# Kernel tuning notes

Hardware: AMD Instinct MI355X
Metric: run time of the kernel (lower is better)

Reference implementation:

```python
import jax, jax.numpy as jnp
import numpy as np

D = 1024
H = 16
HD = D // H


def setup_inputs() -> dict:
    key = jax.random.key(0)
    ks = jax.random.split(key, 13)
    s = 0.02
    inp = {
        "x": jax.random.normal(ks[0], (2, 2048, D), dtype=jnp.float32),
        "Wq": jax.random.normal(ks[1], (D, D), dtype=jnp.float32) * s,
        "bq": jnp.zeros((D,), jnp.float32),
        "Wk": jax.random.normal(ks[2], (D, D), dtype=jnp.float32) * s,
        "bk": jnp.zeros((D,), jnp.float32),
        "Wv": jax.random.normal(ks[3], (D, D), dtype=jnp.float32) * s,
        "bv": jnp.zeros((D,), jnp.float32),
        "Wo": jax.random.normal(ks[4], (D, D), dtype=jnp.float32) * s,
        "bo": jnp.zeros((D,), jnp.float32),
        "W1": jax.random.normal(ks[5], (D, 4 * D), dtype=jnp.float32) * s,
        "b1": jnp.zeros((4 * D,), jnp.float32),
        "W2": jax.random.normal(ks[6], (4 * D, D), dtype=jnp.float32) * s,
        "b2": jnp.zeros((D,), jnp.float32),
    }
    return inp


def reference(x, Wq, bq, Wk, bk, Wv, bv, Wo, bo, W1, b1, W2, b2):
    B, L, _ = x.shape
    # attention (dropout = identity in eval); note: original forward never applies norm1/norm2
    q = (x @ Wq + bq).reshape(B, L, H, HD).transpose(0, 2, 1, 3)  # [B,H,L,HD]
    k = (x @ Wk + bk).reshape(B, L, H, HD).transpose(0, 2, 1, 3)
    v = (x @ Wv + bv).reshape(B, L, H, HD).transpose(0, 2, 1, 3)
    s = jnp.einsum("bhqd,bhkd->bhqk", q, k) / jnp.sqrt(jnp.float32(HD))
    causal = jnp.tril(jnp.ones((L, L), dtype=bool))
    s = jnp.where(causal[None, None, :, :], s, -jnp.inf)
    p = jax.nn.softmax(s, axis=-1)
    y = jnp.einsum("bhqk,bhkd->bhqd", p, v)
    y = y.transpose(0, 2, 1, 3).reshape(B, L, D)
    x = x + (y @ Wo + bo)
    # MLP with SiLU
    h = jax.nn.silu(x @ W1 + b1)
    x = x + (h @ W2 + b2)
    return x
```

## Files before the change

### kernel.cpp

```cpp
#include <hip/hip_runtime.h>
#include <hip/hip_bf16.h>
#include <stdint.h>

using u16 = unsigned short;
typedef __bf16 bf16x8 __attribute__((ext_vector_type(8)));
typedef float f32x4 __attribute__((ext_vector_type(4)));
typedef u16 u16x8 __attribute__((ext_vector_type(8)));

__device__ __forceinline__ float bf2f(u16 u) {
  union { unsigned int i; float f; } v; v.i = ((unsigned int)u) << 16; return v.f;
}
__device__ __forceinline__ u16 f2bf(float f) {
  __bf16 h = (__bf16)f;
  return __builtin_bit_cast(u16, h);
}
__device__ __forceinline__ float fexp2(float x) {
  return __builtin_amdgcn_exp2f(x);
}

__device__ __forceinline__ void gload_lds16(const void* g, void* l) {
  __builtin_amdgcn_global_load_lds(
      (__attribute__((address_space(1))) const void*)g,
      (__attribute__((address_space(3))) void*)l, 16, 0, 0);
}

__global__ void cvt_f32_bf16(const float* __restrict__ in, u16* __restrict__ out) {
  int i = (blockIdx.x * 256 + threadIdx.x) * 8;
  float4 a = *(const float4*)(in + i);
  float4 b = *(const float4*)(in + i + 4);
  u16x8 o;
  o[0] = f2bf(a.x); o[1] = f2bf(a.y); o[2] = f2bf(a.z); o[3] = f2bf(a.w);
  o[4] = f2bf(b.x); o[5] = f2bf(b.y); o[6] = f2bf(b.z); o[7] = f2bf(b.w);
  *(u16x8*)(out + i) = o;
}

__global__ void transpose_cvt(const float* __restrict__ W, u16* __restrict__ Wt,
                              int K, int N) {
  __shared__ float t[32][33];
  const int tx = threadIdx.x & 31, ty = threadIdx.x >> 5;
  const int n0 = blockIdx.x * 32, k0 = blockIdx.y * 32;
#pragma unroll
  for (int i = 0; i < 32; i += 8)
    t[ty + i][tx] = W[(size_t)(k0 + ty + i) * N + n0 + tx];
  __syncthreads();
#pragma unroll
  for (int i = 0; i < 32; i += 8)
    Wt[(size_t)(n0 + ty + i) * K + k0 + tx] = f2bf(t[tx][ty + i]);
}

__global__ void transpose_cvt4(const float* __restrict__ Wa, const float* __restrict__ Wb,
                               const float* __restrict__ Wc, const float* __restrict__ Wd,
                               u16* __restrict__ Da, u16* __restrict__ Db,
                               u16* __restrict__ Dc, u16* __restrict__ Dd) {
  __shared__ float t[32][33];
  const int z = blockIdx.z;
  const float* W = (z == 0) ? Wa : (z == 1) ? Wb : (z == 2) ? Wc : Wd;
  u16* D = (z == 0) ? Da : (z == 1) ? Db : (z == 2) ? Dc : Dd;
  const int tx = threadIdx.x & 31, ty = threadIdx.x >> 5;
  const int n0 = blockIdx.x * 32, k0 = blockIdx.y * 32;
#pragma unroll
  for (int i = 0; i < 32; i += 8)
    t[ty + i][tx] = W[(size_t)(k0 + ty + i) * 1024 + n0 + tx];
  __syncthreads();
#pragma unroll
  for (int i = 0; i < 32; i += 8)
    D[(size_t)(n0 + ty + i) * 1024 + k0 + tx] = f2bf(t[tx][ty + i]);
}

__global__ void transpose_v(const u16* __restrict__ qkv, u16* __restrict__ vt) {
  __shared__ u16 tile[32][34];
  const int tx = threadIdx.x & 31, ty = threadIdx.x >> 5;
  const int kv0 = blockIdx.x * 32, d0 = blockIdx.y * 32;
  const int bh = blockIdx.z, b = bh >> 4, h = bh & 15;
#pragma unroll
  for (int i = 0; i < 32; i += 8)
    tile[ty + i][tx] = qkv[(size_t)(b * 2048 + kv0 + ty + i) * 3072 + 2048 + h * 64 + d0 + tx];
  __syncthreads();
#pragma unroll
  for (int i = 0; i < 32; i += 8)
    vt[((size_t)bh * 64 + d0 + ty + i) * 2048 + kv0 + tx] = tile[tx][ty + i];
}

__global__ void concat_bias(const float* __restrict__ bq, const float* __restrict__ bk,
                            const float* __restrict__ bv, float* __restrict__ o) {
  int i = blockIdx.x * 256 + threadIdx.x;
  o[i] = (i < 1024) ? bq[i] : (i < 2048 ? bk[i - 1024] : bv[i - 2048]);
}

template <int EPI>
__global__ __launch_bounds__(512, 2) void gemm256_kernel(
    const u16* __restrict__ A, const u16* __restrict__ Bt,
    const float* __restrict__ bias, u16* __restrict__ outb,
    int M, int N, int K) {
  __shared__ u16 As[4][8192];
  __shared__ u16 Bs[4][8192];
  const int t = threadIdx.x;
  const int w = t >> 6, lane = t & 63, lr = lane & 15, lg = lane >> 4;
  const int wm = w >> 2, wn = w & 3;
  const int gx = gridDim.x;
  const int nwg = gx * gridDim.y;
  const int p = blockIdx.y * gx + blockIdx.x;
  const int L = (p & 7) * (nwg >> 3) + (p >> 3);
  const int m0 = (L / gx) * 256, n0 = (L % gx) * 256;

  f32x4 acc[8][4] = {};
  bf16x8 bfr[4];
  const int NKT = K >> 5;

  auto stageA = [&](int kt) {
#pragma unroll
    for (int l = 0; l < 2; ++l) {
      int slot = l * 512 + t;
      int row = slot >> 2, cs = slot & 3;
      gload_lds16(&A[(size_t)(m0 + row) * K + kt * 32 + cs * 8], &As[kt & 3][slot * 8]);
    }
  };
  auto stageB = [&](int kt) {
#pragma unroll
    for (int l = 0; l < 2; ++l) {
      int slot = l * 512 + t;
      int row = slot >> 2, cs = slot & 3;
      gload_lds16(&Bt[(size_t)(n0 + row) * K + kt * 32 + cs * 8], &Bs[kt & 3][slot * 8]);
    }
  };

  stageA(0); stageB(0); stageA(1); stageB(1); stageA(2); stageB(2);
  asm volatile("s_waitcnt vmcnt(8)" ::: "memory");
  __builtin_amdgcn_s_barrier();

#define PHASE(Q, STAGE)                                                          \
  {                                                                              \
    const u16* Ab = &As[kt & 3][0];                                              \
    bf16x8 af[4];                                                                \
    _Pragma("unroll") for (int m = 0; m < 4; ++m)                                \
        af[m] = *(const bf16x8*)&Ab[(wm * 128 + ((Q) * 4 + m) * 16 + lr) * 32 +  \
                                    lg * 8];                                     \
    if ((Q) == 0) {                                                              \
      const u16* Bb = &Bs[kt & 3][0];                                            \
      _Pragma("unroll") for (int n = 0; n < 4; ++n)                              \
          bfr[n] = *(const bf16x8*)&Bb[(wn * 64 + n * 16 + lr) * 32 + lg * 8];   \
    }                                                                            \
    STAGE;                                                                       \
    __builtin_amdgcn_s_barrier();                                                \
    asm volatile("s_waitcnt lgkmcnt(0)" ::: "memory");                           \
    __builtin_amdgcn_sched_barrier(0);                                           \
    __builtin_amdgcn_s_setprio(1);                                               \
    _Pragma("unroll") for (int m = 0; m < 4; ++m)                                \
        _Pragma("unroll") for (int n = 0; n < 4; ++n)                            \
            acc[(Q) * 4 + m][n] = __builtin_amdgcn_mfma_f32_16x16x32_bf16(       \
                af[m], bfr[n], acc[(Q) * 4 + m][n], 0, 0, 0);                    \
    __builtin_amdgcn_s_setprio(0);                                               \
  }

  int kt = 0;
  for (; kt < NKT - 3; ++kt) {
    PHASE(0, stageA(kt + 3));
    __builtin_amdgcn_s_barrier();
    PHASE(1, stageB(kt + 3));
    asm volatile("s_waitcnt vmcnt(8)" ::: "memory");
    __builtin_amdgcn_s_barrier();
  }
  asm volatile("s_waitcnt vmcnt(0)" ::: "memory");
  __builtin_amdgcn_s_barrier();
  for (; kt < NKT; ++kt) {
    PHASE(0, (void)0);
    __builtin_amdgcn_s_barrier();
    PHASE(1, (void)0);
    __builtin_amdgcn_s_barrier();
  }
#undef PHASE

#pragma unroll
  for (int mf = 0; mf < 8; ++mf)
#pragma unroll
    for (int nf = 0; nf < 4; ++nf)
#pragma unroll
      for (int i = 0; i < 4; ++i) {
        int gr = m0 + wm * 128 + mf * 16 + lg * 4 + i;
        int gc = n0 + wn * 64 + nf * 16 + lr;
        float v = acc[mf][nf][i] + bias[gc];
        if constexpr (EPI == 1) v = v / (1.f + __expf(-v));
        outb[(size_t)gr * N + gc] = f2bf(v);
      }
}

template <int EPI>
__global__ __launch_bounds__(256) void gemm_nk64_kernel(
    const u16* __restrict__ A, const u16* __restrict__ Bt,
    const float* __restrict__ bias, const float* __restrict__ resid,
    u16* __restrict__ outb, float* __restrict__ outf, int M, int N, int K) {
  __shared__ u16 As[2][128 * 64];
  __shared__ u16 Bs[2][64 * 64];
  const int t = threadIdx.x;
  const int w = t >> 6, lane = t & 63, lr = lane & 15, lg = lane >> 4;
  const int wm = w >> 1, wn = w & 1;
  const int gx = gridDim.x;
  const int nwg = gx * gridDim.y;
  const int p = blockIdx.y * gx + blockIdx.x;
  const int L = (p & 7) * (nwg >> 3) + (p >> 3);
  const int m0 = (L / gx) * 128, n0 = (L % gx) * 64;

  f32x4 acc[4][2] = {};
  const int nt = K >> 6;

  auto stage = [&](int kt, int buf) {
#pragma unroll
    for (int it = 0; it < 4; ++it) {
      int ofs = (it * 256 + t) * 8;
      int row = ofs >> 6, slot = (ofs >> 3) & 7, ss = slot ^ (row & 7);
      gload_lds16(&A[(size_t)(m0 + row) * K + kt * 64 + ss * 8], &As[buf][ofs]);
    }
#pragma unroll
    for (int it = 0; it < 2; ++it) {
      int ofs = (it * 256 + t) * 8;
      int row = ofs >> 6, slot = (ofs >> 3) & 7, ss = slot ^ (row & 7);
      gload_lds16(&Bt[(size_t)(n0 + row) * K + kt * 64 + ss * 8], &Bs[buf][ofs]);
    }
  };

  stage(0, 0);
  __syncthreads();

  for (int kt = 0; kt < nt; ++kt) {
    const int cur = kt & 1;
    if (kt + 1 < nt) stage(kt + 1, cur ^ 1);
#pragma unroll
    for (int kk = 0; kk < 64; kk += 32) {
      const int kcol = kk + lg * 8;
      bf16x8 af[4], bfr[2];
#pragma unroll
      for (int m = 0; m < 4; ++m) {
        int row = wm * 64 + m * 16 + lr;
        int ss = (kcol >> 3) ^ (row & 7);
        af[m] = *(const bf16x8*)&As[cur][row * 64 + ss * 8];
      }
#pragma unroll
      for (int n = 0; n < 2; ++n) {
        int row = wn * 32 + n * 16 + lr;
        int ss = (kcol >> 3) ^ (row & 7);
        bfr[n] = *(const bf16x8*)&Bs[cur][row * 64 + ss * 8];
      }
#pragma unroll
      for (int m = 0; m < 4; ++m)
#pragma unroll
        for (int n = 0; n < 2; ++n)
          acc[m][n] = __builtin_amdgcn_mfma_f32_16x16x32_bf16(af[m], bfr[n],
                                                              acc[m][n], 0, 0, 0);
    }
    __syncthreads();
  }

  const int r0 = m0 + wm * 64, c0 = n0 + wn * 32;
#pragma unroll
  for (int m = 0; m < 4; ++m)
#pragma unroll
    for (int n = 0; n < 2; ++n)
#pragma unroll
      for (int i = 0; i < 4; ++i) {
        int gr = r0 + m * 16 + lg * 4 + i;
        int gc = c0 + n * 16 + lr;
        float v = acc[m][n][i] + bias[gc];
        if constexpr (EPI == 2 || EPI == 3) v += resid[(size_t)gr * N + gc];
        if constexpr (EPI == 2) {
          outf[(size_t)gr * N + gc] = v;
          outb[(size_t)gr * N + gc] = f2bf(v);
        }
        if constexpr (EPI == 3) outf[(size_t)gr * N + gc] = v;
      }
}

__global__ __launch_bounds__(512) void attn_kernel(const u16* __restrict__ qkv,
                                                   const u16* __restrict__ vtg,
                                                   u16* __restrict__ out) {
  __shared__ u16 smem[24576];
  const int t = threadIdx.x, w = t >> 6, lane = t & 63, lr = lane & 15, lg = lane >> 4;
  const int p = blockIdx.y * 16 + blockIdx.x;
  const int L = (p & 7) * 64 + (p >> 3);
  const int qt = 15 - (L & 15), bh = L >> 4, b = bh >> 4, h = bh & 15;
  const int qbw = qt * 128 + w * 16;
  const int jmax_blk = 2 * qt + 1;
  const int jmax_w = 2 * qt + (w >> 2);

  const float QS = 0.18033688011f;
  bf16x8 qf[2];
#pragma unroll
  for (int kc = 0; kc < 2; ++kc) {
    const u16x8 v = *(const u16x8*)&qkv[(size_t)(b * 2048 + qbw + lr) * 3072 +
                                        h * 64 + kc * 32 + lg * 8];
    bf16x8 q;
#pragma unroll
    for (int jj = 0; jj < 8; ++jj) q[jj] = (__bf16)(bf2f(v[jj]) * QS);
    qf[kc] = q;
  }

  f32x4 yacc[4] = {};
  float S = 0.f;

  auto stage = [&](int j, int buf) {
    u16* Kb = smem + buf * 4096;
    u16* Vb = smem + 8192 + buf * 4096;
    int ofs = t * 8;
    int row = ofs >> 6, slot = (ofs >> 3) & 7, ss = slot ^ (row & 7);
    gload_lds16(&qkv[(size_t)(b * 2048 + j * 64 + row) * 3072 + 1024 + h * 64 + ss * 8],
                &Kb[ofs]);
    gload_lds16(&vtg[((size_t)bh * 64 + row) * 2048 + j * 64 + ss * 8],
                &Vb[ofs]);
  };

  stage(0, 0);
  __syncthreads();

  for (int j = 0; j <= jmax_blk; ++j) {
    const int cur = j & 1;
    if (j < jmax_blk) stage(j + 1, cur ^ 1);

    if (j <= jmax_w) {
      const char* Kc = (const char*)(smem + cur * 4096);
      const char* Vc = (const char*)(smem + 8192 + cur * 4096);
      char* Pw = (char*)(smem + 16384 + w * 1024);

      bf16x8 kf[2][4];
#pragma unroll
      for (int kc = 0; kc < 2; ++kc)
#pragma unroll
        for (int n = 0; n < 4; ++n) {
          int row = n * 16 + lr;
          kf[kc][n] = *(const bf16x8*)(Kc + row * 128 +
                                       ((kc * 64 + lg * 16) ^ ((row & 7) << 4)));
        }
      f32x4 s[4] = {};
#pragma unroll
      for (int n = 0; n < 4; ++n)
#pragma unroll
        for (int kc = 0; kc < 2; ++kc)
          s[n] = __builtin_amdgcn_mfma_f32_16x16x32_bf16(kf[kc][n], qf[kc],
                                                         s[n], 0, 0, 0);
      if (j * 64 + 63 > qbw) {
#pragma unroll
        for (int n = 0; n < 4; ++n)
#pragma unroll
          for (int i = 0; i < 4; ++i) {
            int kabs = j * 64 + n * 16 + lg * 4 + i;
            int qabs = qbw + lr;
            if (kabs > qabs) s[n][i] = -1e30f;
          }
      }
      {
        float rs = 0.f;
#pragma unroll
        for (int n = 0; n < 4; ++n)
#pragma unroll
          for (int i = 0; i < 4; ++i) {
            float pv = fexp2(s[n][i]);
            s[n][i] = pv;
            rs += pv;
          }
        S += rs;
        const int qrow = lr, sw = (qrow & 7) << 4;
#pragma unroll
        for (int n = 0; n < 4; ++n) {
          ushort4 ph;
          ph.x = f2bf(s[n][0]); ph.y = f2bf(s[n][1]);
          ph.z = f2bf(s[n][2]); ph.w = f2bf(s[n][3]);
          *(ushort4*)(Pw + qrow * 128 + ((n * 32 + lg * 8) ^ sw)) = ph;
        }
      }
#pragma unroll
      for (int kc = 0; kc < 2; ++kc) {
        bf16x8 pa, vtf[4];
        {
          int qrow = lr;
          pa = *(const bf16x8*)(Pw + qrow * 128 +
                                ((kc * 64 + lg * 16) ^ ((qrow & 7) << 4)));
        }
#pragma unroll
        for (int n = 0; n < 4; ++n) {
          int row = n * 16 + lr;
          vtf[n] = *(const bf16x8*)(Vc + row * 128 +
                                    ((kc * 64 + lg * 16) ^ ((row & 7) << 4)));
        }
#pragma unroll
        for (int n = 0; n < 4; ++n)
          yacc[n] = __builtin_amdgcn_mfma_f32_16x16x32_bf16(pa, vtf[n],
                                                            yacc[n], 0, 0, 0);
      }
    }
    __syncthreads();
  }

  {
    float Sv = S;
    Sv += __shfl_xor(Sv, 16, 64);
    Sv += __shfl_xor(Sv, 32, 64);
    float inv = 1.f / Sv;
#pragma unroll
    for (int i = 0; i < 4; ++i) {
      float ivq = __shfl(inv, lg * 4 + i, 64);
#pragma unroll
      for (int n = 0; n < 4; ++n) {
        int row = b * 2048 + qbw + lg * 4 + i;
        int col = h * 64 + n * 16 + lr;
        out[(size_t)row * 1024 + col] = f2bf(yacc[n][i] * ivq);
      }
    }
  }
}

extern "C" void kernel_launch(void* const* d_in, const int* in_sizes, int n_in,
                              void* d_out, int out_size, void* d_ws, size_t ws_size,
                              hipStream_t stream) {
  const float* x  = (const float*)d_in[0];
  const float* Wq = (const float*)d_in[1];
  const float* bq = (const float*)d_in[2];
  const float* Wk = (const float*)d_in[3];
  const float* bk = (const float*)d_in[4];
  const float* Wv = (const float*)d_in[5];
  const float* bv = (const float*)d_in[6];
  const float* Wo = (const float*)d_in[7];
  const float* bo = (const float*)d_in[8];
  const float* W1 = (const float*)d_in[9];
  const float* b1 = (const float*)d_in[10];
  const float* W2 = (const float*)d_in[11];
  const float* b2 = (const float*)d_in[12];
  float* out = (float*)d_out;

  char* ws = (char*)d_ws;
  const size_t MB = 1u << 20;
  u16*   xb    = (u16*)(ws + 0);
  u16*   wtqkv = (u16*)(ws + 8 * MB);
  u16*   wto   = (u16*)(ws + 14 * MB);
  u16*   wt1   = (u16*)(ws + 16 * MB);
  u16*   wt2   = (u16*)(ws + 24 * MB);
  float* bqkv  = (float*)(ws + 32 * MB);
  u16*   qkv   = (u16*)(ws + 33 * MB);
  u16*   attn  = (u16*)(ws + 57 * MB);
  float* x2f   = (float*)(ws + 65 * MB);
  u16*   x2b   = (u16*)(ws + 81 * MB);
  u16*   hbuf  = (u16*)(ws + 89 * MB);
  u16*   vtg   = xb;

  cvt_f32_bf16<<<2048, 256, 0, stream>>>(x, xb);
  transpose_cvt4<<<dim3(32, 32, 4), 256, 0, stream>>>(
      Wq, Wk, Wv, Wo, wtqkv, wtqkv + 1024 * 1024, wtqkv + 2 * 1024 * 1024, wto);
  transpose_cvt<<<dim3(128, 32), 256, 0, stream>>>(W1, wt1, 1024, 4096);
  transpose_cvt<<<dim3(32, 128), 256, 0, stream>>>(W2, wt2, 4096, 1024);
  concat_bias<<<12, 256, 0, stream>>>(bq, bk, bv, bqkv);

  gemm256_kernel<0><<<dim3(12, 16), 512, 0, stream>>>(
      xb, wtqkv, bqkv, qkv, 4096, 3072, 1024);
  transpose_v<<<dim3(64, 2, 32), 256, 0, stream>>>(qkv, vtg);
  attn_kernel<<<dim3(16, 32), 512, 0, stream>>>(qkv, vtg, attn);
  gemm_nk64_kernel<2><<<dim3(16, 32), 256, 0, stream>>>(
      attn, wto, bo, x, x2b, x2f, 4096, 1024, 1024);
  gemm256_kernel<1><<<dim3(16, 16), 512, 0, stream>>>(
      x2b, wt1, b1, hbuf, 4096, 4096, 1024);
  gemm_nk64_kernel<3><<<dim3(16, 32), 256, 0, stream>>>(
      hbuf, wt2, b2, x2f, nullptr, out, 4096, 1024, 4096);
}
```

Baseline: 223.5 us.

## Replace final MLP down-projection with split-K 256x256 GEMM using atomic accumulation

The W2 projection (K=4096, N=1024) moves from a 128x64-tile kernel to a 256x256-tile kernel split four ways along K, with a 4-stage LDS pipeline and fp32 atomicAdd into the output. The Wo GEMM now writes the residual plus b2 straight into the final output as the initial value, which removes the separate x2f buffer. The aim is better MFMA tile reuse and enough blocks to fill the GPU on the long-K GEMM. The cost is atomic traffic, nondeterministic summation order, and a dependency on the earlier kernel having initialised the output.

```diff
diff --git a/kernel.cpp b/kernel.cpp
--- a/kernel.cpp
+++ b/kernel.cpp
@@ -184,11 +184,108 @@
       }
 }
 
-template <int EPI>
+__global__ __launch_bounds__(512, 2) void gemm256_splitk(
+    const u16* __restrict__ A, const u16* __restrict__ Bt,
+    float* __restrict__ out, int M, int N, int Ktot) {
+  __shared__ u16 As[4][8192];
+  __shared__ u16 Bs[4][8192];
+  const int t = threadIdx.x;
+  const int w = t >> 6, lane = t & 63, lr = lane & 15, lg = lane >> 4;
+  const int wm = w >> 2, wn = w & 3;
+  const int gx = gridDim.x;
+  const int nwg = gx * gridDim.y;
+  const int p = blockIdx.y * gx + blockIdx.x;
+  const int L = (p & 7) * (nwg >> 3) + (p >> 3);
+  const int m0 = (L / gx) * 256, n0 = (L % gx) * 256;
+  const int KS = Ktot >> 2;
+  const int kbase = blockIdx.z * KS;
+
+  f32x4 acc[8][4] = {};
+  bf16x8 bfr[4];
+  const int NKT = KS >> 5;
+
+  auto stageA = [&](int kt) {
+#pragma unroll
+    for (int l = 0; l < 2; ++l) {
+      int slot = l * 512 + t;
+      int row = slot >> 2, cs = slot & 3;
+      gload_lds16(&A[(size_t)(m0 + row) * Ktot + kbase + kt * 32 + cs * 8],
+                  &As[kt & 3][slot * 8]);
+    }
+  };
+  auto stageB = [&](int kt) {
+#pragma unroll
+    for (int l = 0; l < 2; ++l) {
+      int slot = l * 512 + t;
+      int row = slot >> 2, cs = slot & 3;
+      gload_lds16(&Bt[(size_t)(n0 + row) * Ktot + kbase + kt * 32 + cs * 8],
+                  &Bs[kt & 3][slot * 8]);
+    }
+  };
+
+  stageA(0); stageB(0); stageA(1); stageB(1); stageA(2); stageB(2);
+  asm volatile("s_waitcnt vmcnt(8)" ::: "memory");
+  __builtin_amdgcn_s_barrier();
+
+#define PHASE(Q, STAGE)                                                          \
+  {                                                                              \
+    const u16* Ab = &As[kt & 3][0];                                              \
+    bf16x8 af[4];                                                                \
+    _Pragma("unroll") for (int m = 0; m < 4; ++m)                                \
+        af[m] = *(const bf16x8*)&Ab[(wm * 128 + ((Q) * 4 + m) * 16 + lr) * 32 +  \
+                                    lg * 8];                                     \
+    if ((Q) == 0) {                                                              \
+      const u16* Bb = &Bs[kt & 3][0];                                            \
+      _Pragma("unroll") for (int n = 0; n < 4; ++n)                              \
+          bfr[n] = *(const bf16x8*)&Bb[(wn * 64 + n * 16 + lr) * 32 + lg * 8];   \
+    }                                                                            \
+    STAGE;                                                                       \
+    __builtin_amdgcn_s_barrier();                                                \
+    asm volatile("s_waitcnt lgkmcnt(0)" ::: "memory");                           \
+    __builtin_amdgcn_sched_barrier(0);                                           \
+    __builtin_amdgcn_s_setprio(1);                                               \
+    _Pragma("unroll") for (int m = 0; m < 4; ++m)                                \
+        _Pragma("unroll") for (int n = 0; n < 4; ++n)                            \
+            acc[(Q) * 4 + m][n] = __builtin_amdgcn_mfma_f32_16x16x32_bf16(       \
+                af[m], bfr[n], acc[(Q) * 4 + m][n], 0, 0, 0);                    \
+    __builtin_amdgcn_s_setprio(0);                                               \
+  }
+
+  int kt = 0;
+  for (; kt < NKT - 3; ++kt) {
+    PHASE(0, stageA(kt + 3));
+    __builtin_amdgcn_s_barrier();
+    PHASE(1, stageB(kt + 3));
+    asm volatile("s_waitcnt vmcnt(8)" ::: "memory");
+    __builtin_amdgcn_s_barrier();
+  }
+  asm volatile("s_waitcnt vmcnt(0)" ::: "memory");
+  __builtin_amdgcn_s_barrier();
+  for (; kt < NKT; ++kt) {
+    PHASE(0, (void)0);
+    __builtin_amdgcn_s_barrier();
+    PHASE(1, (void)0);
+    __builtin_amdgcn_s_barrier();
+  }
+#undef PHASE
+
+#pragma unroll
+  for (int mf = 0; mf < 8; ++mf)
+#pragma unroll
+    for (int nf = 0; nf < 4; ++nf)
+#pragma unroll
+      for (int i = 0; i < 4; ++i) {
+        int gr = m0 + wm * 128 + mf * 16 + lg * 4 + i;
+        int gc = n0 + wn * 64 + nf * 16 + lr;
+        atomicAdd(&out[(size_t)gr * N + gc], acc[mf][nf][i]);
+      }
+}
+
 __global__ __launch_bounds__(256) void gemm_nk64_kernel(
     const u16* __restrict__ A, const u16* __restrict__ Bt,
     const float* __restrict__ bias, const float* __restrict__ resid,
-    u16* __restrict__ outb, float* __restrict__ outf, int M, int N, int K) {
+    u16* __restrict__ outb, const float* __restrict__ bias2,
+    float* __restrict__ outinit, int M, int N, int K) {
   __shared__ u16 As[2][128 * 64];
   __shared__ u16 Bs[2][64 * 64];
   const int t = threadIdx.x;
@@ -259,13 +356,9 @@
       for (int i = 0; i < 4; ++i) {
         int gr = r0 + m * 16 + lg * 4 + i;
         int gc = c0 + n * 16 + lr;
-        float v = acc[m][n][i] + bias[gc];
-        if constexpr (EPI == 2 || EPI == 3) v += resid[(size_t)gr * N + gc];
-        if constexpr (EPI == 2) {
-          outf[(size_t)gr * N + gc] = v;
-          outb[(size_t)gr * N + gc] = f2bf(v);
-        }
-        if constexpr (EPI == 3) outf[(size_t)gr * N + gc] = v;
+        float v = acc[m][n][i] + bias[gc] + resid[(size_t)gr * N + gc];
+        outb[(size_t)gr * N + gc] = f2bf(v);
+        outinit[(size_t)gr * N + gc] = v + bias2[gc];
       }
 }
 
@@ -434,7 +527,6 @@
   float* bqkv  = (float*)(ws + 32 * MB);
   u16*   qkv   = (u16*)(ws + 33 * MB);
   u16*   attn  = (u16*)(ws + 57 * MB);
-  float* x2f   = (float*)(ws + 65 * MB);
   u16*   x2b   = (u16*)(ws + 81 * MB);
   u16*   hbuf  = (u16*)(ws + 89 * MB);
   u16*   vtg   = xb;
@@ -450,10 +542,10 @@
       xb, wtqkv, bqkv, qkv, 4096, 3072, 1024);
   transpose_v<<<dim3(64, 2, 32), 256, 0, stream>>>(qkv, vtg);
   attn_kernel<<<dim3(16, 32), 512, 0, stream>>>(qkv, vtg, attn);
-  gemm_nk64_kernel<2><<<dim3(16, 32), 256, 0, stream>>>(
-      attn, wto, bo, x, x2b, x2f, 4096, 1024, 1024);
+  gemm_nk64_kernel<<<dim3(16, 32), 256, 0, stream>>>(
+      attn, wto, bo, x, x2b, b2, out, 4096, 1024, 1024);
   gemm256_kernel<1><<<dim3(16, 16), 512, 0, stream>>>(
       x2b, wt1, b1, hbuf, 4096, 4096, 1024);
-  gemm_nk64_kernel<3><<<dim3(16, 32), 256, 0, stream>>>(
-      hbuf, wt2, b2, x2f, nullptr, out, 4096, 1024, 4096);
-}
+  gemm256_splitk<<<dim3(4, 16, 4), 512, 0, stream>>>(
+      hbuf, wt2, out, 4096, 1024, 4096);
+}
```

After: 250.2 us. 1.12x slower.
